# Kernel tuning notes

Measured on AMD Instinct MI355X. Metric: run time of the kernel, lower is better.

## Reference

```python
import jax, jax.numpy as jnp
import numpy as np

WIN = (4, 4, 4)
SHIFT = (2, 2, 2)
HEADS = 6


def _rel_index(win):
    H, W, D = win
    coords = np.stack(np.meshgrid(np.arange(H), np.arange(W), np.arange(D), indexing='ij'))
    cf = coords.reshape(3, -1)
    rel = (cf[:, :, None] - cf[:, None, :]).transpose(1, 2, 0)
    rel[..., 0] += H - 1
    rel[..., 1] += W - 1
    rel[..., 2] += D - 1
    rel[..., 0] *= (2 * W - 1) * (2 * D - 1)
    rel[..., 1] *= 2 * D - 1
    return rel.sum(-1)  # [N, N] int


def _attn_mask(shape, win, shift):
    H, W, D = shape
    wh, ww, wd = win
    mask = np.zeros((H, W, D))
    cnt = 0
    for h in (slice(0, -wh), slice(-wh, -shift[0]), slice(-shift[0], None)):
        for w in (slice(0, -ww), slice(-ww, -shift[1]), slice(-shift[1], None)):
            for d in (slice(0, -wd), slice(-wd, -shift[2]), slice(-shift[2], None)):
                mask[h, w, d] = cnt
                cnt += 1
    m = mask.reshape(H // wh, wh, W // ww, ww, D // wd, wd)
    m = m.transpose(0, 2, 4, 1, 3, 5).reshape(-1, wh * ww * wd)  # [nW, N]
    am = m[:, None, :] - m[:, :, None]
    return np.where(am != 0, -100.0, 0.0).astype(np.float32)  # [nW, N, N]


def _win_part(x, win):
    B, H, W, D, C = x.shape
    wh, ww, wd = win
    x = x.reshape(B, H // wh, wh, W // ww, ww, D // wd, wd, C)
    x = x.transpose(0, 1, 3, 5, 2, 4, 6, 7)
    return x.reshape(-1, wh * ww * wd, C)


def _win_rev(wins, win, shape):
    B, H, W, D, C = shape
    wh, ww, wd = win
    x = wins.reshape(B, H // wh, W // ww, D // wd, wh, ww, wd, C)
    x = x.transpose(0, 1, 4, 2, 5, 3, 6, 7)
    return x.reshape(B, H, W, D, C)


def _ln(x, g, b):
    m = x.mean(-1, keepdims=True)
    v = ((x - m) ** 2).mean(-1, keepdims=True)
    return (x - m) / jnp.sqrt(v + 1e-5) * g + b


def setup_inputs() -> dict:
    key = jax.random.key(0)
    ks = jax.random.split(key, 8)
    C, Hd = 192, 768
    s = 0.02
    return {
        'x': jax.random.normal(ks[0], (2, 32, 32, 32, C), jnp.float32),
        'g1': jnp.ones((C,), jnp.float32),
        'b1': jnp.zeros((C,), jnp.float32),
        'wqkv': jax.random.normal(ks[1], (C, 3 * C), jnp.float32) * s,
        'bqkv': jnp.zeros((3 * C,), jnp.float32),
        'wo': jax.random.normal(ks[2], (C, C), jnp.float32) * s,
        'bo': jnp.zeros((C,), jnp.float32),
        'bias_table': jax.random.normal(ks[3], (343, HEADS), jnp.float32) * s,
        'g2': jnp.ones((C,), jnp.float32),
        'b2': jnp.zeros((C,), jnp.float32),
        'w1': jax.random.normal(ks[4], (C, Hd), jnp.float32) * s,
        'bm1': jnp.zeros((Hd,), jnp.float32),
        'w2': jax.random.normal(ks[5], (Hd, C), jnp.float32) * s,
        'bm2': jnp.zeros((C,), jnp.float32),
    }


def reference(x, g1, b1, wqkv, bqkv, wo, bo, bias_table, g2, b2, w1, bm1, w2, bm2):
    B, H, W, D, C = x.shape
    hd = C // HEADS
    N = WIN[0] * WIN[1] * WIN[2]
    rel_idx = _rel_index(WIN)  # static numpy
    mask = jnp.asarray(_attn_mask((H, W, D), WIN, SHIFT))  # [nW, N, N]

    residual = x
    xn = _ln(x, g1, b1)
    # cyclic shift (dims divisible by window -> no padding needed)
    sx = jnp.roll(xn, (-SHIFT[0], -SHIFT[1], -SHIFT[2]), axis=(1, 2, 3))
    xw = _win_part(sx, WIN)  # [B*nW, N, C]
    B_ = xw.shape[0]
    nW = B_ // B

    qkv = (xw @ wqkv + bqkv).reshape(B_, N, 3, HEADS, hd).transpose(2, 0, 3, 1, 4)
    q, k, v = qkv[0], qkv[1], qkv[2]  # [B_, h, N, hd]
    attn = jnp.einsum('bhid,bhjd->bhij', q, k) * (hd ** -0.5)
    bias = bias_table[rel_idx.reshape(-1)].reshape(N, N, HEADS).transpose(2, 0, 1)
    attn = attn + bias[None]
    attn = attn.reshape(B, nW, HEADS, N, N) + mask[None, :, None]
    attn = jax.nn.softmax(attn.reshape(B_, HEADS, N, N), axis=-1)
    out = jnp.einsum('bhij,bhjd->bhid', attn, v).transpose(0, 2, 1, 3).reshape(B_, N, C)
    out = out @ wo + bo

    sx = _win_rev(out, WIN, (B, H, W, D, C))
    xs = jnp.roll(sx, (SHIFT[0], SHIFT[1], SHIFT[2]), axis=(1, 2, 3))
    xo = residual + xs
    h1 = jax.nn.gelu(_ln(xo, g2, b2) @ w1 + bm1, approximate=False)
    return xo + (h1 @ w2 + bm2)
```

## Files before the change

kernel.cpp:

```cpp
#include <hip/hip_runtime.h>
#include <math.h>

typedef unsigned short u16;
typedef unsigned int   u32;
using short8  = __attribute__((ext_vector_type(8))) short;
using float4v = __attribute__((ext_vector_type(4))) float;

__device__ __forceinline__ float b2f(u16 u){ return __uint_as_float(((u32)u)<<16); }
__device__ __forceinline__ u16 f2b(float f){
  u32 x = __float_as_uint(f);
  x += 0x7FFFu + ((x>>16)&1u);
  return (u16)(x>>16);
}

__device__ __forceinline__ u32 cvtpk_bf16(float lo, float hi){
  u32 r; asm("v_cvt_pk_bf16_f32 %0, %1, %2" : "=v"(r) : "v"(lo), "v"(hi));
  return r;
}

__device__ __forceinline__ void gload_lds16(const u16* g, u16* l){
  __builtin_amdgcn_global_load_lds((const __attribute__((address_space(1))) void*)g,
                                   (__attribute__((address_space(3))) void*)l, 16, 0, 0);
}

__device__ __forceinline__ float gelu_t(float x){
  float x2 = x*x;
  float z  = x * __builtin_fmaf(-0.1029434f, x2, -2.3022077f);
  float e  = __builtin_amdgcn_exp2f(z);
  return x * __builtin_amdgcn_rcpf(1.f + e);
}

__global__ void transpose_all(const float* __restrict__ wqkv, const float* __restrict__ wo,
                              const float* __restrict__ w1,   const float* __restrict__ w2,
                              u16* __restrict__ wqkvT, u16* __restrict__ woT,
                              u16* __restrict__ w1P,   u16* __restrict__ w2P){
  int idx = blockIdx.x*256 + threadIdx.x;
  if (idx < 110592){ int r=idx/576, c=idx-r*576; wqkvT[c*192+r]=f2b(wqkv[idx]); }
  else if (idx < 147456){ int j=idx-110592; int r=j/192, c=j-r*192; woT[c*192+r]=f2b(wo[j]); }
  else if (idx < 294912){
    int j = idx-147456;
    int tile = j >> 9, w = j & 511;
    int e = w & 7, l16 = (w>>3)&15, quad = w>>7;
    int hc = (tile/6)*16 + l16, k = (tile%6)*32 + quad*8 + e;
    w1P[j] = f2b(w1[k*768 + hc]);
  } else if (idx < 442368){
    int j = idx-294912;
    int tile = j >> 9, w = j & 511;
    int e = w & 7, l16 = (w>>3)&15, quad = w>>7;
    int oc = (tile/24)*16 + l16, k = (tile%24)*32 + quad*8 + e;
    w2P[j] = f2b(w2[k*192 + oc]);
  }
}

__global__ __launch_bounds__(256) void ln_kernel(const float* __restrict__ x,
    const float* __restrict__ g, const float* __restrict__ bvec,
    u16* __restrict__ out)
{
  int wave = threadIdx.x >> 6, lane = threadIdx.x & 63;
  int token = blockIdx.x*4 + wave;
  int b = token >> 15, r = token & 32767;
  int hs = r >> 10, ws = (r >> 5) & 31, ds = r & 31;
  int h = (hs+2)&31, w = (ws+2)&31, d = (ds+2)&31;
  int src = ((b*32 + h)*32 + w)*32 + d;
  int win = ((b*8 + (hs>>2))*8 + (ws>>2))*8 + (ds>>2);
  int n   = ((hs&3)*4 + (ws&3))*4 + (ds&3);
  int dst = win*64 + n;
  float v[3];
  #pragma unroll
  for (int t=0;t<3;t++) v[t] = x[(size_t)src*192 + lane + t*64];
  float s  = v[0]+v[1]+v[2];
  float s2 = v[0]*v[0]+v[1]*v[1]+v[2]*v[2];
  #pragma unroll
  for (int o=32;o>=1;o>>=1){ s += __shfl_xor(s,o); s2 += __shfl_xor(s2,o); }
  float mean = s*(1.0f/192.0f);
  float var  = s2*(1.0f/192.0f) - mean*mean;
  float rstd = rsqrtf(var + 1e-5f);
  #pragma unroll
  for (int t=0;t<3;t++){
    int c = lane + t*64;
    out[(size_t)dst*192 + c] = f2b((v[t]-mean)*rstd*g[c] + bvec[c]);
  }
}

template<int MODE, int NB>
__global__ __launch_bounds__(256) void gemm_fk(
    const u16* __restrict__ A, const u16* __restrict__ BT, const float* __restrict__ bias,
    const int K, const int N,
    u16* __restrict__ outb, float* __restrict__ outf, const float* __restrict__ resf)
{
  __shared__ u16 As[64*192];
  __shared__ u16 Bs[64*192];
  const int lin = blockIdx.x;
  const int xcd = lin & 7, idx = lin >> 3;
  const int mb = idx / NB, nb = idx - mb*NB;
  const int m0 = (xcd*128 + mb) * 64, n0 = nb * 64;
  const int tid = threadIdx.x;
  const int wv = tid >> 6, lane = tid & 63;
  const int quad = lane >> 4, l16 = lane & 15;
  const int wm = (wv >> 1) * 32, wn = (wv & 1) * 32;

  float4v acc[2][2];
  #pragma unroll
  for (int a=0;a<2;a++) for (int b=0;b<2;b++) acc[a][b] = (float4v){0.f,0.f,0.f,0.f};

  const int srow8 = lane >> 3;
  const int scc   = (lane & 7) ^ srow8;
  const int c3x   = l16 & 7;

  for (int kc = 0; kc < K; kc += 192){
    #pragma unroll
    for (int t=0;t<6;t++){
      int ig = wv*6 + t;
      int g = ig >> 3, ro = ig & 7;
      int row = ro*8 + srow8;
      gload_lds16(A  + (size_t)(m0+row)*K + kc + g*64 + scc*8, As + g*4096 + ro*512);
      gload_lds16(BT + (size_t)(n0+row)*K + kc + g*64 + scc*8, Bs + g*4096 + ro*512);
    }
    __syncthreads();
    #pragma unroll
    for (int ks=0; ks<6; ks++){
      const int cc = ks*4 + quad, g = cc >> 3, c3 = (cc & 7) ^ c3x;
      short8 af[2], bf2[2];
      #pragma unroll
      for (int mt=0;mt<2;mt++) af[mt]  = *(const short8*)(As + g*4096 + (wm+mt*16+l16)*64 + c3*8);
      #pragma unroll
      for (int nt=0;nt<2;nt++) bf2[nt] = *(const short8*)(Bs + g*4096 + (wn+nt*16+l16)*64 + c3*8);
      #pragma unroll
      for (int mt=0;mt<2;mt++)
        #pragma unroll
        for (int nt=0;nt<2;nt++)
          acc[mt][nt] = __builtin_amdgcn_mfma_f32_16x16x32_bf16(af[mt], bf2[nt], acc[mt][nt], 0,0,0);
    }
    if (kc + 192 < K) __syncthreads();
  }

  #pragma unroll
  for (int nt=0;nt<2;nt++){
    int col = n0 + wn + nt*16 + l16;
    float bv = bias[col];
    #pragma unroll
    for (int mt=0;mt<2;mt++){
      float4v a = acc[mt][nt];
      #pragma unroll
      for (int r=0;r<4;r++){
        int mrow = m0 + wm + mt*16 + quad*4 + r;
        float v = a[r] + bv;
        if (MODE == 4){
          if (col < 192) v *= 0.17677669529663687f;
          outb[(size_t)mrow*N + col] = f2b(v);
        } else {
          int win = mrow >> 6, n = mrow & 63;
          int b = win >> 9, rw = win & 511;
          int hs = ((rw>>6)&7)*4 + (n>>4);
          int ws = ((rw>>3)&7)*4 + ((n>>2)&3);
          int ds = (rw&7)*4 + (n&3);
          int h=(hs+2)&31, w=(ws+2)&31, d=(ds+2)&31;
          size_t t = (size_t)((b*32+h)*32+w)*32 + d;
          outf[t*192 + col] = v + resf[t*192 + col];
        }
      }
    }
  }
}

__global__ __launch_bounds__(256) void mlp_fused(
    const float* __restrict__ xo, const float* __restrict__ g2, const float* __restrict__ b2,
    const u16* __restrict__ w1P, const float* __restrict__ bm1,
    const u16* __restrict__ w2P, const float* __restrict__ bm2,
    float* __restrict__ out)
{
  __shared__ u16 S[2*32*192];
  u16* Ash = S;
  u16* Hsh = S + 32*192;
  const int tid = threadIdx.x;
  const int wv = tid >> 6, lane = tid & 63;
  const int quad = lane >> 4, l16 = lane & 15;
  const int tok0 = blockIdx.x * 32;
  const int c3x = l16 & 7;

  {
    float gg[3], bb[3];
    #pragma unroll
    for (int t=0;t<3;t++){ gg[t] = g2[lane+t*64]; bb[t] = b2[lane+t*64]; }
    #pragma unroll
    for (int tt=0;tt<8;tt++){
      const int tl = wv*8 + tt;
      const float* row = xo + (size_t)(tok0+tl)*192;
      float v[3];
      #pragma unroll
      for (int t=0;t<3;t++) v[t] = row[lane + t*64];
      float s = v[0]+v[1]+v[2];
      float s2 = v[0]*v[0]+v[1]*v[1]+v[2]*v[2];
      #pragma unroll
      for (int o=32;o>=1;o>>=1){ s += __shfl_xor(s,o); s2 += __shfl_xor(s2,o); }
      float mean = s*(1.0f/192.0f);
      float rstd = rsqrtf(s2*(1.0f/192.0f) - mean*mean + 1e-5f);
      const int slot = ((lane>>3) ^ (tl&7));
      #pragma unroll
      for (int t=0;t<3;t++)
        Ash[t*2048 + tl*64 + slot*8 + (lane&7)] = f2b((v[t]-mean)*rstd*gg[t] + bb[t]);
    }
  }
  __syncthreads();

  const int mb = wv*3;
  float4v dacc[3][2];
  #pragma unroll
  for (int a=0;a<3;a++) for (int b=0;b<2;b++) dacc[a][b] = (float4v){0.f,0.f,0.f,0.f};

  for (int p=0; p<4; p++){
    if (p) __syncthreads();
    float4v acc[3][2];
    #pragma unroll
    for (int a=0;a<3;a++) for (int b=0;b<2;b++) acc[a][b] = (float4v){0.f,0.f,0.f,0.f};
    #pragma unroll
    for (int ks=0; ks<6; ks++){
      const int cc = ks*4 + quad, g = cc >> 3, c3 = (cc & 7) ^ c3x;
      short8 bf[2], af[3];
      #pragma unroll
      for (int ntl=0;ntl<2;ntl++)
        bf[ntl] = *(const short8*)(Ash + g*2048 + (ntl*16+l16)*64 + c3*8);
      #pragma unroll
      for (int mtl=0;mtl<3;mtl++)
        af[mtl] = *(const short8*)(w1P + ((size_t)((p*12 + mb + mtl)*6 + ks)*64 + lane)*8);
      #pragma unroll
      for (int mtl=0;mtl<3;mtl++)
        #pragma unroll
        for (int ntl=0;ntl<2;ntl++)
          acc[mtl][ntl] = __builtin_amdgcn_mfma_f32_16x16x32_bf16(af[mtl], bf[ntl], acc[mtl][ntl], 0,0,0);
    }
    #pragma unroll
    for (int mtl=0;mtl<3;mtl++){
      const int hl0 = (mb+mtl)*16 + quad*4;
      const float4v bv = *(const float4v*)(bm1 + p*192 + hl0);
      const int g = hl0 >> 3, sub = hl0 & 7;
      #pragma unroll
      for (int ntl=0;ntl<2;ntl++){
        const int tok = ntl*16 + l16;
        union { unsigned long long d; u32 w[2]; } pk;
        pk.w[0] = cvtpk_bf16(gelu_t(acc[mtl][ntl][0] + bv[0]), gelu_t(acc[mtl][ntl][1] + bv[1]));
        pk.w[1] = cvtpk_bf16(gelu_t(acc[mtl][ntl][2] + bv[2]), gelu_t(acc[mtl][ntl][3] + bv[3]));
        *(unsigned long long*)(Hsh + tok*192 + ((g ^ (tok&7))<<3) + sub) = pk.d;
      }
    }
    __syncthreads();
    #pragma unroll
    for (int ks=0; ks<6; ks++){
      const int g = ks*4 + quad;
      short8 bf[2], af[3];
      #pragma unroll
      for (int ntl=0;ntl<2;ntl++){
        const int tok = ntl*16 + l16;
        bf[ntl] = *(const short8*)(Hsh + tok*192 + ((g ^ (tok&7))<<3));
      }
      #pragma unroll
      for (int mtl=0;mtl<3;mtl++)
        af[mtl] = *(const short8*)(w2P + ((size_t)((mb+mtl)*24 + p*6 + ks)*64 + lane)*8);
      #pragma unroll
      for (int mtl=0;mtl<3;mtl++)
        #pragma unroll
        for (int ntl=0;ntl<2;ntl++)
          dacc[mtl][ntl] = __builtin_amdgcn_mfma_f32_16x16x32_bf16(af[mtl], bf[ntl], dacc[mtl][ntl], 0,0,0);
    }
  }
  __syncthreads();

  float4v* F = (float4v*)S;
  #pragma unroll
  for (int mtl=0;mtl<3;mtl++){
    const int oc0 = (mb+mtl)*16 + quad*4;
    const float4v bv = *(const float4v*)(bm2 + oc0);
    #pragma unroll
    for (int ntl=0;ntl<2;ntl++){
      const int tok = ntl*16 + l16;
      float4v o;
      #pragma unroll
      for (int r=0;r<4;r++) o[r] = dacc[mtl][ntl][r] + bv[r];
      F[tok*48 + ((oc0>>2) ^ (tok&7))] = o;
    }
  }
  __syncthreads();
  const float4v* xo4 = (const float4v*)(xo + (size_t)tok0*192);
  float4v* out4 = (float4v*)(out + (size_t)tok0*192);
  #pragma unroll
  for (int it=0; it<6; it++){
    int f = it*256 + tid;
    int tok = f/48, c = f - tok*48;
    float4v v = F[tok*48 + (c ^ (tok&7))];
    float4v xv = xo4[f];
    #pragma unroll
    for (int r=0;r<4;r++) v[r] += xv[r];
    out4[f] = v;
  }
}

__global__ __launch_bounds__(192,3) void attn_mfma(
    const u16* __restrict__ qkv, const float* __restrict__ bias_table,
    u16* __restrict__ out)
{
  __shared__ u16  Psh [3][64*72];
  __shared__ u16  VTsh[3][32*72];
  __shared__ float bsh[3][344];
  const int win  = blockIdx.x >> 1;
  const int wv   = threadIdx.x / 64;
  const int lane = threadIdx.x & 63;
  const int hg   = (blockIdx.x & 1)*3 + wv;
  const int quad = lane >> 4, l16 = lane & 15;

  u16* P  = &Psh[wv][0];
  u16* VT = &VTsh[wv][0];
  float* bs = &bsh[wv][0];
  const u16* base = qkv + (size_t)win*64*576 + hg*32;

  for (int idx = lane; idx < 343; idx += 64) bs[idx] = bias_table[idx*6 + hg];

  {
    const int a = (lane & 15)*4 + (lane >> 4);
    #pragma unroll
    for (int t=0;t<4;t++){
      union { uint4 v; u16 u[8]; } vv;
      vv.v = *(const uint4*)(base + (size_t)lane*576 + 384 + t*8);
      #pragma unroll
      for (int e=0;e<8;e++) VT[(t*8+e)*72 + a] = vv.u[e];
    }
  }

  short8 qf[4], kf[4];
  #pragma unroll
  for (int mt=0;mt<4;mt++) qf[mt] = *(const short8*)(base + (size_t)(mt*16 + l16)*576 + quad*8);
  #pragma unroll
  for (int nt=0;nt<4;nt++) kf[nt] = *(const short8*)(base + (size_t)(nt*16 + l16)*576 + 192 + quad*8);

  float4v s[4][4];
  #pragma unroll
  for (int mt=0;mt<4;mt++)
    #pragma unroll
    for (int nt=0;nt<4;nt++)
      s[mt][nt] = __builtin_amdgcn_mfma_f32_16x16x32_bf16(qf[mt], kf[nt], (float4v){0.f,0.f,0.f,0.f}, 0,0,0);

  const int rwn = win & 511;
  const int bh=(rwn>>6)&7, bw=(rwn>>3)&7, bd=rwn&7;
  const int jw = l16>>2, jd = l16&3;
  const int gw_j = (bw==7) ? ((jw  <2)?3:6) : 0;
  const int gd_j = (bd==7) ? ((jd  <2)?1:2) : 0;
  const int gw_i = (bw==7) ? ((quad<2)?3:6) : 0;
  const int laneoff = (quad - jw)*7 - jd + 171;
  #pragma unroll
  for (int mt=0;mt<4;mt++){
    const int gh_i = (bh==7) ? ((mt<2)?9:18) : 0;
    #pragma unroll
    for (int nt=0;nt<4;nt++){
      const int gh_j = (bh==7) ? ((nt<2)?9:18) : 0;
      const int bb = (mt-nt)*49 + laneoff;
      #pragma unroll
      for (int r=0;r<4;r++){
        const int gd_i = (bd==7) ? ((r<2)?1:2) : 0;
        float sv = s[mt][nt][r] + bs[bb + r];
        if ((gh_i + gw_i + gd_i) != (gh_j + gw_j + gd_j)) sv -= 100.f;
        s[mt][nt][r] = sv;
      }
    }
  }

  #pragma unroll
  for (int mt=0;mt<4;mt++){
    #pragma unroll
    for (int r=0;r<4;r++){
      float m0 = fmaxf(fmaxf(s[mt][0][r], s[mt][1][r]), fmaxf(s[mt][2][r], s[mt][3][r]));
      #pragma unroll
      for (int o=8;o>=1;o>>=1) m0 = fmaxf(m0, __shfl_xor(m0,o));
      float sum = 0.f;
      float e[4];
      #pragma unroll
      for (int nt=0;nt<4;nt++){ e[nt] = __expf(s[mt][nt][r] - m0); sum += e[nt]; }
      #pragma unroll
      for (int o=8;o>=1;o>>=1) sum += __shfl_xor(sum,o);
      const float rinv = __builtin_amdgcn_rcpf(sum);
      union { unsigned long long d; u32 w[2]; } pk;
      pk.w[0] = cvtpk_bf16(e[0]*rinv, e[1]*rinv);
      pk.w[1] = cvtpk_bf16(e[2]*rinv, e[3]*rinv);
      *(unsigned long long*)(&P[(mt*16 + quad*4 + r)*72 + l16*4]) = pk.d;
    }
  }

  float4v o2[4][2];
  #pragma unroll
  for (int mt=0;mt<4;mt++){ o2[mt][0]=(float4v){0.f,0.f,0.f,0.f}; o2[mt][1]=(float4v){0.f,0.f,0.f,0.f}; }
  #pragma unroll
  for (int s2=0;s2<2;s2++){
    short8 vfrag[2];
    #pragma unroll
    for (int ct=0;ct<2;ct++) vfrag[ct] = *(const short8*)(&VT[(ct*16 + l16)*72 + s2*32 + quad*8]);
    #pragma unroll
    for (int mt=0;mt<4;mt++){
      short8 pfrag = *(const short8*)(&P[(mt*16 + l16)*72 + s2*32 + quad*8]);
      #pragma unroll
      for (int ct=0;ct<2;ct++)
        o2[mt][ct] = __builtin_amdgcn_mfma_f32_16x16x32_bf16(pfrag, vfrag[ct], o2[mt][ct], 0,0,0);
    }
  }

  #pragma unroll
  for (int mt=0;mt<4;mt++)
    #pragma unroll
    for (int ct=0;ct<2;ct++)
      #pragma unroll
      for (int r=0;r<4;r++){
        int i = mt*16 + quad*4 + r;
        out[((size_t)win*64 + i)*192 + hg*32 + ct*16 + l16] = f2b(o2[mt][ct][r]);
      }
}

extern "C" void kernel_launch(void* const* d_in, const int* in_sizes, int n_in,
                              void* d_out, int out_size, void* d_ws, size_t ws_size,
                              hipStream_t stream)
{
  const float* x    = (const float*)d_in[0];
  const float* g1   = (const float*)d_in[1];
  const float* b1   = (const float*)d_in[2];
  const float* wqkv = (const float*)d_in[3];
  const float* bqkv = (const float*)d_in[4];
  const float* wo   = (const float*)d_in[5];
  const float* bo   = (const float*)d_in[6];
  const float* btab = (const float*)d_in[7];
  const float* g2   = (const float*)d_in[8];
  const float* b2v  = (const float*)d_in[9];
  const float* w1   = (const float*)d_in[10];
  const float* bm1  = (const float*)d_in[11];
  const float* w2   = (const float*)d_in[12];
  const float* bm2  = (const float*)d_in[13];
  float* out = (float*)d_out;

  char* ws = (char*)d_ws;
  u16*  wqkvT = (u16*)(ws + 0);
  u16*  woT   = (u16*)(ws + 221184);
  u16*  w1P   = (u16*)(ws + 294912);
  u16*  w2P   = (u16*)(ws + 589824);
  u16*  xw    = (u16*)(ws + 1048576);
  u16*  qkvb  = (u16*)(ws + 26214400);
  float* xo   = (float*)(ws + 26214400);

  transpose_all<<<1728,256,0,stream>>>(wqkv, wo, w1, w2, wqkvT, woT, w1P, w2P);

  ln_kernel<<<16384,256,0,stream>>>(x, g1, b1, xw);
  gemm_fk<4,9><<<9216,256,0,stream>>>(xw, wqkvT, bqkv, 192, 576, qkvb, nullptr, nullptr);
  attn_mfma<<<2048,192,0,stream>>>(qkvb, btab, xw);
  gemm_fk<2,3><<<3072,256,0,stream>>>(xw, woT, bo, 192, 192, nullptr, xo, x);
  mlp_fused<<<2048,256,0,stream>>>(xo, g2, b2v, w1P, bm1, w2P, bm2, out);
}
```

Measured before the change: 281.0 us.

## Reuse A tile across N tiles in GEMM and software-pipeline MLP up/down GEMMs

The projection GEMM now keeps one A tile in LDS and loops over several N tiles, double-buffering the B tile so the next weight slice loads while the current one is multiplied. This cuts redundant A loads and the number of blocks. The fused MLP kernel double-buffers the hidden activations, interleaving the up-projection of chunk p with the down-projection of chunk p-1, which removes one barrier per chunk. The costs are more LDS per block, more live registers (launch bounds now target 4 blocks), and fewer blocks in flight for the GEMMs.

```diff
diff --git a/kernel.cpp b/kernel.cpp
--- a/kernel.cpp
+++ b/kernel.cpp
@@ -82,41 +82,50 @@
   }
 }
 
-template<int MODE, int NB>
+template<int MODE, int NBG, int NT>
 __global__ __launch_bounds__(256) void gemm_fk(
     const u16* __restrict__ A, const u16* __restrict__ BT, const float* __restrict__ bias,
     const int K, const int N,
     u16* __restrict__ outb, float* __restrict__ outf, const float* __restrict__ resf)
 {
   __shared__ u16 As[64*192];
-  __shared__ u16 Bs[64*192];
+  __shared__ u16 Bs[2][64*192];
   const int lin = blockIdx.x;
   const int xcd = lin & 7, idx = lin >> 3;
-  const int mb = idx / NB, nb = idx - mb*NB;
-  const int m0 = (xcd*128 + mb) * 64, n0 = nb * 64;
+  const int mb = idx / NBG, nbg = idx - mb*NBG;
+  const int m0 = (xcd*128 + mb) * 64;
   const int tid = threadIdx.x;
   const int wv = tid >> 6, lane = tid & 63;
   const int quad = lane >> 4, l16 = lane & 15;
   const int wm = (wv >> 1) * 32, wn = (wv & 1) * 32;
-
-  float4v acc[2][2];
-  #pragma unroll
-  for (int a=0;a<2;a++) for (int b=0;b<2;b++) acc[a][b] = (float4v){0.f,0.f,0.f,0.f};
-
   const int srow8 = lane >> 3;
   const int scc   = (lane & 7) ^ srow8;
   const int c3x   = l16 & 7;
 
-  for (int kc = 0; kc < K; kc += 192){
-    #pragma unroll
-    for (int t=0;t<6;t++){
-      int ig = wv*6 + t;
-      int g = ig >> 3, ro = ig & 7;
-      int row = ro*8 + srow8;
-      gload_lds16(A  + (size_t)(m0+row)*K + kc + g*64 + scc*8, As + g*4096 + ro*512);
-      gload_lds16(BT + (size_t)(n0+row)*K + kc + g*64 + scc*8, Bs + g*4096 + ro*512);
-    }
+  #pragma unroll
+  for (int t=0;t<6;t++){
+    int ig = wv*6 + t, g = ig >> 3, ro = ig & 7, row = ro*8 + srow8;
+    gload_lds16(A  + (size_t)(m0+row)*K + g*64 + scc*8, As + g*4096 + ro*512);
+    gload_lds16(BT + (size_t)(nbg*NT*64+row)*K + g*64 + scc*8, Bs[0] + g*4096 + ro*512);
+  }
+
+  #pragma unroll
+  for (int nt2=0; nt2<NT; nt2++){
     __syncthreads();
+    if (nt2+1 < NT){
+      #pragma unroll
+      for (int t=0;t<6;t++){
+        int ig = wv*6 + t, g = ig >> 3, ro = ig & 7, row = ro*8 + srow8;
+        gload_lds16(BT + (size_t)((nbg*NT+nt2+1)*64+row)*K + g*64 + scc*8,
+                    Bs[(nt2+1)&1] + g*4096 + ro*512);
+      }
+    }
+    const u16* Bc = Bs[nt2&1];
+
+    float4v acc[2][2];
+    #pragma unroll
+    for (int a=0;a<2;a++) for (int b=0;b<2;b++) acc[a][b] = (float4v){0.f,0.f,0.f,0.f};
+
     #pragma unroll
     for (int ks=0; ks<6; ks++){
       const int cc = ks*4 + quad, g = cc >> 3, c3 = (cc & 7) ^ c3x;
@@ -124,54 +133,55 @@
       #pragma unroll
       for (int mt=0;mt<2;mt++) af[mt]  = *(const short8*)(As + g*4096 + (wm+mt*16+l16)*64 + c3*8);
       #pragma unroll
-      for (int nt=0;nt<2;nt++) bf2[nt] = *(const short8*)(Bs + g*4096 + (wn+nt*16+l16)*64 + c3*8);
+      for (int nt=0;nt<2;nt++) bf2[nt] = *(const short8*)(Bc + g*4096 + (wn+nt*16+l16)*64 + c3*8);
       #pragma unroll
       for (int mt=0;mt<2;mt++)
         #pragma unroll
         for (int nt=0;nt<2;nt++)
           acc[mt][nt] = __builtin_amdgcn_mfma_f32_16x16x32_bf16(af[mt], bf2[nt], acc[mt][nt], 0,0,0);
     }
-    if (kc + 192 < K) __syncthreads();
-  }
-
-  #pragma unroll
-  for (int nt=0;nt<2;nt++){
-    int col = n0 + wn + nt*16 + l16;
-    float bv = bias[col];
-    #pragma unroll
-    for (int mt=0;mt<2;mt++){
-      float4v a = acc[mt][nt];
-      #pragma unroll
-      for (int r=0;r<4;r++){
-        int mrow = m0 + wm + mt*16 + quad*4 + r;
-        float v = a[r] + bv;
-        if (MODE == 4){
-          if (col < 192) v *= 0.17677669529663687f;
-          outb[(size_t)mrow*N + col] = f2b(v);
-        } else {
-          int win = mrow >> 6, n = mrow & 63;
-          int b = win >> 9, rw = win & 511;
-          int hs = ((rw>>6)&7)*4 + (n>>4);
-          int ws = ((rw>>3)&7)*4 + ((n>>2)&3);
-          int ds = (rw&7)*4 + (n&3);
-          int h=(hs+2)&31, w=(ws+2)&31, d=(ds+2)&31;
-          size_t t = (size_t)((b*32+h)*32+w)*32 + d;
-          outf[t*192 + col] = v + resf[t*192 + col];
+
+    const int n0 = (nbg*NT + nt2)*64;
+    #pragma unroll
+    for (int nt=0;nt<2;nt++){
+      int col = n0 + wn + nt*16 + l16;
+      float bv = bias[col];
+      #pragma unroll
+      for (int mt=0;mt<2;mt++){
+        float4v a = acc[mt][nt];
+        #pragma unroll
+        for (int r=0;r<4;r++){
+          int mrow = m0 + wm + mt*16 + quad*4 + r;
+          float v = a[r] + bv;
+          if (MODE == 4){
+            if (col < 192) v *= 0.17677669529663687f;
+            outb[(size_t)mrow*N + col] = f2b(v);
+          } else {
+            int win = mrow >> 6, n = mrow & 63;
+            int b = win >> 9, rw = win & 511;
+            int hs = ((rw>>6)&7)*4 + (n>>4);
+            int ws = ((rw>>3)&7)*4 + ((n>>2)&3);
+            int ds = (rw&7)*4 + (n&3);
+            int h=(hs+2)&31, w=(ws+2)&31, d=(ds+2)&31;
+            size_t t = (size_t)((b*32+h)*32+w)*32 + d;
+            outf[t*192 + col] = v + resf[t*192 + col];
+          }
         }
       }
     }
   }
 }
 
-__global__ __launch_bounds__(256) void mlp_fused(
+__global__ __launch_bounds__(256,4) void mlp_fused(
     const float* __restrict__ xo, const float* __restrict__ g2, const float* __restrict__ b2,
     const u16* __restrict__ w1P, const float* __restrict__ bm1,
     const u16* __restrict__ w2P, const float* __restrict__ bm2,
     float* __restrict__ out)
 {
-  __shared__ u16 S[2*32*192];
-  u16* Ash = S;
-  u16* Hsh = S + 32*192;
+  __shared__ u16 S[3*32*192];
+  u16* Ash  = S;
+  u16* Hsh0 = S + 6144;
+  u16* Hsh1 = S + 12288;
   const int tid = threadIdx.x;
   const int wv = tid >> 6, lane = tid & 63;
   const int quad = lane >> 4, l16 = lane & 15;
@@ -207,28 +217,9 @@
   float4v dacc[3][2];
   #pragma unroll
   for (int a=0;a<3;a++) for (int b=0;b<2;b++) dacc[a][b] = (float4v){0.f,0.f,0.f,0.f};
-
-  for (int p=0; p<4; p++){
-    if (p) __syncthreads();
-    float4v acc[3][2];
-    #pragma unroll
-    for (int a=0;a<3;a++) for (int b=0;b<2;b++) acc[a][b] = (float4v){0.f,0.f,0.f,0.f};
-    #pragma unroll
-    for (int ks=0; ks<6; ks++){
-      const int cc = ks*4 + quad, g = cc >> 3, c3 = (cc & 7) ^ c3x;
-      short8 bf[2], af[3];
-      #pragma unroll
-      for (int ntl=0;ntl<2;ntl++)
-        bf[ntl] = *(const short8*)(Ash + g*2048 + (ntl*16+l16)*64 + c3*8);
-      #pragma unroll
-      for (int mtl=0;mtl<3;mtl++)
-        af[mtl] = *(const short8*)(w1P + ((size_t)((p*12 + mb + mtl)*6 + ks)*64 + lane)*8);
-      #pragma unroll
-      for (int mtl=0;mtl<3;mtl++)
-        #pragma unroll
-        for (int ntl=0;ntl<2;ntl++)
-          acc[mtl][ntl] = __builtin_amdgcn_mfma_f32_16x16x32_bf16(af[mtl], bf[ntl], acc[mtl][ntl], 0,0,0);
-    }
+  float4v acc[3][2];
+
+  auto GELU_STORE = [&](int p, u16* HshW){
     #pragma unroll
     for (int mtl=0;mtl<3;mtl++){
       const int hl0 = (mb+mtl)*16 + quad*4;
@@ -240,30 +231,89 @@
         union { unsigned long long d; u32 w[2]; } pk;
         pk.w[0] = cvtpk_bf16(gelu_t(acc[mtl][ntl][0] + bv[0]), gelu_t(acc[mtl][ntl][1] + bv[1]));
         pk.w[1] = cvtpk_bf16(gelu_t(acc[mtl][ntl][2] + bv[2]), gelu_t(acc[mtl][ntl][3] + bv[3]));
-        *(unsigned long long*)(Hsh + tok*192 + ((g ^ (tok&7))<<3) + sub) = pk.d;
+        *(unsigned long long*)(HshW + tok*192 + ((g ^ (tok&7))<<3) + sub) = pk.d;
       }
     }
-    __syncthreads();
+  };
+
+  #pragma unroll
+  for (int a=0;a<3;a++) for (int b=0;b<2;b++) acc[a][b] = (float4v){0.f,0.f,0.f,0.f};
+  #pragma unroll
+  for (int ks=0; ks<6; ks++){
+    const int cc = ks*4 + quad, g = cc >> 3, c3 = (cc & 7) ^ c3x;
+    short8 bfU[2], afU[3];
+    #pragma unroll
+    for (int ntl=0;ntl<2;ntl++)
+      bfU[ntl] = *(const short8*)(Ash + g*2048 + (ntl*16+l16)*64 + c3*8);
+    #pragma unroll
+    for (int mtl=0;mtl<3;mtl++)
+      afU[mtl] = *(const short8*)(w1P + ((size_t)((mb + mtl)*6 + ks)*64 + lane)*8);
+    #pragma unroll
+    for (int mtl=0;mtl<3;mtl++)
+      #pragma unroll
+      for (int ntl=0;ntl<2;ntl++)
+        acc[mtl][ntl] = __builtin_amdgcn_mfma_f32_16x16x32_bf16(afU[mtl], bfU[ntl], acc[mtl][ntl], 0,0,0);
+  }
+  GELU_STORE(0, Hsh0);
+  __syncthreads();
+
+  for (int p=1; p<4; p++){
+    u16* HshR = ((p-1)&1) ? Hsh1 : Hsh0;
+    u16* HshW = (p&1)     ? Hsh1 : Hsh0;
+    #pragma unroll
+    for (int a=0;a<3;a++) for (int b=0;b<2;b++) acc[a][b] = (float4v){0.f,0.f,0.f,0.f};
     #pragma unroll
     for (int ks=0; ks<6; ks++){
-      const int g = ks*4 + quad;
-      short8 bf[2], af[3];
+      const int cc = ks*4 + quad, g = cc >> 3, c3 = (cc & 7) ^ c3x;
+      const int gd = ks*4 + quad;
+      short8 bfU[2], afU[3], bfD[2], afD[3];
+      #pragma unroll
+      for (int ntl=0;ntl<2;ntl++)
+        bfU[ntl] = *(const short8*)(Ash + g*2048 + (ntl*16+l16)*64 + c3*8);
       #pragma unroll
       for (int ntl=0;ntl<2;ntl++){
         const int tok = ntl*16 + l16;
-        bf[ntl] = *(const short8*)(Hsh + tok*192 + ((g ^ (tok&7))<<3));
+        bfD[ntl] = *(const short8*)(HshR + tok*192 + ((gd ^ (tok&7))<<3));
       }
       #pragma unroll
       for (int mtl=0;mtl<3;mtl++)
-        af[mtl] = *(const short8*)(w2P + ((size_t)((mb+mtl)*24 + p*6 + ks)*64 + lane)*8);
+        afU[mtl] = *(const short8*)(w1P + ((size_t)((p*12 + mb + mtl)*6 + ks)*64 + lane)*8);
+      #pragma unroll
+      for (int mtl=0;mtl<3;mtl++)
+        afD[mtl] = *(const short8*)(w2P + ((size_t)((mb + mtl)*24 + (p-1)*6 + ks)*64 + lane)*8);
       #pragma unroll
       for (int mtl=0;mtl<3;mtl++)
         #pragma unroll
         for (int ntl=0;ntl<2;ntl++)
-          dacc[mtl][ntl] = __builtin_amdgcn_mfma_f32_16x16x32_bf16(af[mtl], bf[ntl], dacc[mtl][ntl], 0,0,0);
-    }
-  }
-  __syncthreads();
+          acc[mtl][ntl]  = __builtin_amdgcn_mfma_f32_16x16x32_bf16(afU[mtl], bfU[ntl], acc[mtl][ntl], 0,0,0);
+      #pragma unroll
+      for (int mtl=0;mtl<3;mtl++)
+        #pragma unroll
+        for (int ntl=0;ntl<2;ntl++)
+          dacc[mtl][ntl] = __builtin_amdgcn_mfma_f32_16x16x32_bf16(afD[mtl], bfD[ntl], dacc[mtl][ntl], 0,0,0);
+    }
+    GELU_STORE(p, HshW);
+    __syncthreads();
+  }
+
+  #pragma unroll
+  for (int ks=0; ks<6; ks++){
+    const int gd = ks*4 + quad;
+    short8 bfD[2], afD[3];
+    #pragma unroll
+    for (int ntl=0;ntl<2;ntl++){
+      const int tok = ntl*16 + l16;
+      bfD[ntl] = *(const short8*)(Hsh1 + tok*192 + ((gd ^ (tok&7))<<3));
+    }
+    #pragma unroll
+    for (int mtl=0;mtl<3;mtl++)
+      afD[mtl] = *(const short8*)(w2P + ((size_t)((mb + mtl)*24 + 18 + ks)*64 + lane)*8);
+    #pragma unroll
+    for (int mtl=0;mtl<3;mtl++)
+      #pragma unroll
+      for (int ntl=0;ntl<2;ntl++)
+        dacc[mtl][ntl] = __builtin_amdgcn_mfma_f32_16x16x32_bf16(afD[mtl], bfD[ntl], dacc[mtl][ntl], 0,0,0);
+  }
 
   float4v* F = (float4v*)S;
   #pragma unroll
@@ -443,8 +493,8 @@
   transpose_all<<<1728,256,0,stream>>>(wqkv, wo, w1, w2, wqkvT, woT, w1P, w2P);
 
   ln_kernel<<<16384,256,0,stream>>>(x, g1, b1, xw);
-  gemm_fk<4,9><<<9216,256,0,stream>>>(xw, wqkvT, bqkv, 192, 576, qkvb, nullptr, nullptr);
+  gemm_fk<4,3,3><<<3072,256,0,stream>>>(xw, wqkvT, bqkv, 192, 576, qkvb, nullptr, nullptr);
   attn_mfma<<<2048,192,0,stream>>>(qkvb, btab, xw);
-  gemm_fk<2,3><<<3072,256,0,stream>>>(xw, woT, bo, 192, 192, nullptr, xo, x);
+  gemm_fk<2,1,3><<<1024,256,0,stream>>>(xw, woT, bo, 192, 192, nullptr, xo, x);
   mlp_fused<<<2048,256,0,stream>>>(xo, g2, b2v, w1P, bm1, w2P, bm2, out);
 }
```

New measurement: 296.3 us. 1.05x slower.

## Double-buffer MLP hidden tile and overlap second GEMM with next first GEMM

Applied to the files above, without the earlier changes.

In the fused MLP kernel, the hidden activation tile in shared memory is now double-buffered, and the p-loop is software-pipelined. The second GEMM for chunk p-1 runs in the same iteration as the first GEMM for chunk p, and the last chunk is drained after the loop. This removes one block-wide barrier per chunk and gives the scheduler independent MFMA and load work to interleave. In exchange, LDS use per block grows by half, which can reduce how many blocks fit on a compute unit.

```diff
diff --git a/kernel.cpp b/kernel.cpp
--- a/kernel.cpp
+++ b/kernel.cpp
@@ -169,9 +169,10 @@
     const u16* __restrict__ w2P, const float* __restrict__ bm2,
     float* __restrict__ out)
 {
-  __shared__ u16 S[2*32*192];
-  u16* Ash = S;
-  u16* Hsh = S + 32*192;
+  __shared__ u16 S[3*32*192];
+  u16* Ash  = S;
+  u16* Hsh0 = S + 6144;
+  u16* Hsh1 = S + 12288;
   const int tid = threadIdx.x;
   const int wv = tid >> 6, lane = tid & 63;
   const int quad = lane >> 4, l16 = lane & 15;
@@ -208,27 +209,52 @@
   #pragma unroll
   for (int a=0;a<3;a++) for (int b=0;b<2;b++) dacc[a][b] = (float4v){0.f,0.f,0.f,0.f};
 
+  #pragma unroll
   for (int p=0; p<4; p++){
-    if (p) __syncthreads();
+    u16* HshW = (p&1) ? Hsh1 : Hsh0;
+    u16* HshR = (p&1) ? Hsh0 : Hsh1;
+
     float4v acc[3][2];
     #pragma unroll
     for (int a=0;a<3;a++) for (int b=0;b<2;b++) acc[a][b] = (float4v){0.f,0.f,0.f,0.f};
     #pragma unroll
     for (int ks=0; ks<6; ks++){
       const int cc = ks*4 + quad, g = cc >> 3, c3 = (cc & 7) ^ c3x;
-      short8 bf[2], af[3];
+      short8 bfU[2], afU[3];
       #pragma unroll
       for (int ntl=0;ntl<2;ntl++)
-        bf[ntl] = *(const short8*)(Ash + g*2048 + (ntl*16+l16)*64 + c3*8);
+        bfU[ntl] = *(const short8*)(Ash + g*2048 + (ntl*16+l16)*64 + c3*8);
       #pragma unroll
       for (int mtl=0;mtl<3;mtl++)
-        af[mtl] = *(const short8*)(w1P + ((size_t)((p*12 + mb + mtl)*6 + ks)*64 + lane)*8);
+        afU[mtl] = *(const short8*)(w1P + ((size_t)((p*12 + mb + mtl)*6 + ks)*64 + lane)*8);
       #pragma unroll
       for (int mtl=0;mtl<3;mtl++)
         #pragma unroll
         for (int ntl=0;ntl<2;ntl++)
-          acc[mtl][ntl] = __builtin_amdgcn_mfma_f32_16x16x32_bf16(af[mtl], bf[ntl], acc[mtl][ntl], 0,0,0);
-    }
+          acc[mtl][ntl] = __builtin_amdgcn_mfma_f32_16x16x32_bf16(afU[mtl], bfU[ntl], acc[mtl][ntl], 0,0,0);
+    }
+
+    if (p > 0){
+      #pragma unroll
+      for (int ks=0; ks<6; ks++){
+        const int gd = ks*4 + quad;
+        short8 bfD[2], afD[3];
+        #pragma unroll
+        for (int ntl=0;ntl<2;ntl++){
+          const int tok = ntl*16 + l16;
+          bfD[ntl] = *(const short8*)(HshR + tok*192 + ((gd ^ (tok&7))<<3));
+        }
+        #pragma unroll
+        for (int mtl=0;mtl<3;mtl++)
+          afD[mtl] = *(const short8*)(w2P + ((size_t)((mb + mtl)*24 + (p-1)*6 + ks)*64 + lane)*8);
+        #pragma unroll
+        for (int mtl=0;mtl<3;mtl++)
+          #pragma unroll
+          for (int ntl=0;ntl<2;ntl++)
+            dacc[mtl][ntl] = __builtin_amdgcn_mfma_f32_16x16x32_bf16(afD[mtl], bfD[ntl], dacc[mtl][ntl], 0,0,0);
+      }
+    }
+
     #pragma unroll
     for (int mtl=0;mtl<3;mtl++){
       const int hl0 = (mb+mtl)*16 + quad*4;
@@ -240,30 +266,30 @@
         union { unsigned long long d; u32 w[2]; } pk;
         pk.w[0] = cvtpk_bf16(gelu_t(acc[mtl][ntl][0] + bv[0]), gelu_t(acc[mtl][ntl][1] + bv[1]));
         pk.w[1] = cvtpk_bf16(gelu_t(acc[mtl][ntl][2] + bv[2]), gelu_t(acc[mtl][ntl][3] + bv[3]));
-        *(unsigned long long*)(Hsh + tok*192 + ((g ^ (tok&7))<<3) + sub) = pk.d;
+        *(unsigned long long*)(HshW + tok*192 + ((g ^ (tok&7))<<3) + sub) = pk.d;
       }
     }
     __syncthreads();
-    #pragma unroll
-    for (int ks=0; ks<6; ks++){
-      const int g = ks*4 + quad;
-      short8 bf[2], af[3];
-      #pragma unroll
-      for (int ntl=0;ntl<2;ntl++){
-        const int tok = ntl*16 + l16;
-        bf[ntl] = *(const short8*)(Hsh + tok*192 + ((g ^ (tok&7))<<3));
-      }
-      #pragma unroll
-      for (int mtl=0;mtl<3;mtl++)
-        af[mtl] = *(const short8*)(w2P + ((size_t)((mb+mtl)*24 + p*6 + ks)*64 + lane)*8);
-      #pragma unroll
-      for (int mtl=0;mtl<3;mtl++)
-        #pragma unroll
-        for (int ntl=0;ntl<2;ntl++)
-          dacc[mtl][ntl] = __builtin_amdgcn_mfma_f32_16x16x32_bf16(af[mtl], bf[ntl], dacc[mtl][ntl], 0,0,0);
-    }
-  }
-  __syncthreads();
+  }
+
+  #pragma unroll
+  for (int ks=0; ks<6; ks++){
+    const int gd = ks*4 + quad;
+    short8 bfD[2], afD[3];
+    #pragma unroll
+    for (int ntl=0;ntl<2;ntl++){
+      const int tok = ntl*16 + l16;
+      bfD[ntl] = *(const short8*)(Hsh1 + tok*192 + ((gd ^ (tok&7))<<3));
+    }
+    #pragma unroll
+    for (int mtl=0;mtl<3;mtl++)
+      afD[mtl] = *(const short8*)(w2P + ((size_t)((mb + mtl)*24 + 18 + ks)*64 + lane)*8);
+    #pragma unroll
+    for (int mtl=0;mtl<3;mtl++)
+      #pragma unroll
+      for (int ntl=0;ntl<2;ntl++)
+        dacc[mtl][ntl] = __builtin_amdgcn_mfma_f32_16x16x32_bf16(afD[mtl], bfD[ntl], dacc[mtl][ntl], 0,0,0);
+  }
 
   float4v* F = (float4v*)S;
   #pragma unroll
```

New measurement: 293.9 us. 1.05x slower.
